# Kernel optimization log

Measured on AMD Instinct MI355X. Metric: run time of the kernel, lower is better.

Reference implementation:

```python
import jax, jax.numpy as jnp
import numpy as np

N = 150000   # nodes
E = 600000   # edges
F_IN = 32    # node features
H = 128      # hidden_channels == MLP_neurons
G = 2048     # graphs in batch


def setup_inputs() -> dict:
    key = jax.random.key(0)
    ks = iter(jax.random.split(key, 40))
    inp = {}
    inp['x'] = jax.random.normal(next(ks), (N, F_IN), dtype=jnp.float32)
    inp['edge_index'] = jax.random.randint(next(ks), (2, E), 0, N)
    inp['batch'] = jnp.sort(jax.random.randint(next(ks), (N,), 0, G))
    # GINConv MLPs: Linear(in,H) ReLU Linear(H,H) ReLU Linear(H,H)
    for i, f_in in enumerate([F_IN, H, H]):
        s1 = 1.0 / np.sqrt(f_in)
        s2 = 1.0 / np.sqrt(H)
        inp[f'c{i}_w1'] = jax.random.uniform(next(ks), (f_in, H), minval=-s1, maxval=s1)
        inp[f'c{i}_b1'] = jnp.zeros((H,), jnp.float32)
        inp[f'c{i}_w2'] = jax.random.uniform(next(ks), (H, H), minval=-s2, maxval=s2)
        inp[f'c{i}_b2'] = jnp.zeros((H,), jnp.float32)
        inp[f'c{i}_w3'] = jax.random.uniform(next(ks), (H, H), minval=-s2, maxval=s2)
        inp[f'c{i}_b3'] = jnp.zeros((H,), jnp.float32)
    s = 1.0 / np.sqrt(H)
    inp['fc0_w'] = jax.random.uniform(next(ks), (H, H), minval=-s, maxval=s)
    inp['fc0_b'] = jnp.zeros((H,), jnp.float32)
    inp['fc1_w'] = jax.random.uniform(next(ks), (H, H), minval=-s, maxval=s)
    inp['fc1_b'] = jnp.zeros((H,), jnp.float32)
    inp['out_w'] = jax.random.uniform(next(ks), (H, 2), minval=-s, maxval=s)
    inp['out_b'] = jnp.zeros((2,), jnp.float32)
    return inp


def _gin_layer(x, edge_index, w1, b1, w2, b2, w3, b3):
    # GINConv with eps=0: h = MLP(x + sum_{j in N(i)} x_j)
    agg = jax.ops.segment_sum(x[edge_index[0]], edge_index[1], num_segments=N)
    h = x + agg
    h = jax.nn.relu(h @ w1 + b1)
    h = jax.nn.relu(h @ w2 + b2)
    h = h @ w3 + b3
    return jax.nn.relu(h)  # outer .relu() in forward


def reference(x, edge_index, batch,
              c0_w1, c0_b1, c0_w2, c0_b2, c0_w3, c0_b3,
              c1_w1, c1_b1, c1_w2, c1_b2, c1_w3, c1_b3,
              c2_w1, c2_b1, c2_w2, c2_b2, c2_w3, c2_b3,
              fc0_w, fc0_b, fc1_w, fc1_b, out_w, out_b):
    h = _gin_layer(x, edge_index, c0_w1, c0_b1, c0_w2, c0_b2, c0_w3, c0_b3)
    h = _gin_layer(h, edge_index, c1_w1, c1_b1, c1_w2, c1_b2, c1_w3, c1_b3)
    h = _gin_layer(h, edge_index, c2_w1, c2_b1, c2_w2, c2_b2, c2_w3, c2_b3)
    # global_mean_pool over graph ids
    sums = jax.ops.segment_sum(h, batch, num_segments=G)            # [G,H]
    cnts = jax.ops.segment_sum(jnp.ones((N,), h.dtype), batch, num_segments=G)
    g = sums / jnp.maximum(cnts, 1.0)[:, None]
    # classifier head (dropout is identity at inference)
    g = jax.nn.relu(g @ fc0_w + fc0_b)
    g = jax.nn.relu(g @ fc1_w + fc1_b)
    return g @ out_w + out_b  # [G,2]
```

## Files before the change

kernel.cpp:

```cpp
#include <hip/hip_runtime.h>
#include <hip/hip_bf16.h>

#define NN 150000
#define EE 600000
#define F_IN 32
#define HD 128
#define GG 2048
#define CAP 28
#define NP 150016

typedef __attribute__((ext_vector_type(8))) short bf16x8;
typedef __attribute__((ext_vector_type(4))) float f32x4;

__device__ inline void split_bf16(float v, unsigned short& hi, unsigned short& lo) {
    __hip_bfloat16 h = __float2bfloat16(v);
    float hv = __bfloat162float(h);
    __hip_bfloat16 l = __float2bfloat16(v - hv);
    hi = *reinterpret_cast<unsigned short*>(&h);
    lo = *reinterpret_cast<unsigned short*>(&l);
}
__device__ inline unsigned short bf16_hi(float v) {
    __hip_bfloat16 h = __float2bfloat16(v);
    return *reinterpret_cast<unsigned short*>(&h);
}
__device__ inline float bf2f(unsigned short u) {
    union { unsigned int i; float f; } c;
    c.i = ((unsigned int)u) << 16;
    return c.f;
}

__global__ void init_zero(int* __restrict__ cnt_node, float* __restrict__ pooled) {
    int i = blockIdx.x * blockDim.x + threadIdx.x;
    if (i < NN) cnt_node[i] = 0;
    if (i < GG * HD) pooled[i] = 0.f;
}

__global__ void build_graph(const int* __restrict__ ei,
                            int* __restrict__ cnt_node,
                            int* __restrict__ bucket) {
    int e = blockIdx.x * blockDim.x + threadIdx.x;
    if (e >= EE) return;
    int src = ei[e];
    int dst = ei[EE + e];
    int slot = atomicAdd(&cnt_node[dst], 1);
    if (slot < CAP) bucket[dst * CAP + slot] = src;
}

struct PrepDesc { const float* src; unsigned short* dhi; unsigned short* dlo; int K; };
struct PrepArgs { PrepDesc d[9]; };

__global__ void prep_weights(PrepArgs pa) {
    PrepDesc de = pa.d[blockIdx.y];
    int total = de.K * HD;
    int KS = de.K >> 5;
    for (int idx = blockIdx.x * blockDim.x + threadIdx.x; idx < total;
         idx += gridDim.x * blockDim.x) {
        int k = idx / HD, h = idx - (idx / HD) * HD;
        unsigned short hi, lo;
        split_bf16(de.src[idx], hi, lo);
        int nt = h >> 4, m = h & 15;
        int ks = k >> 5, quad = (k >> 3) & 3, e = k & 7;
        int lane = quad * 16 + m;
        int pidx = ((nt * KS + ks) * 64 + lane) * 8 + e;
        de.dhi[pidx] = hi;
        de.dlo[pidx] = lo;
    }
}

template <int K_IN, bool BF16IN, bool POOL>
__launch_bounds__(128, 3)
__global__ void gin_layer(const void* __restrict__ hin_,
                          const int* __restrict__ cnt_node,
                          const int* __restrict__ bucket,
                          const unsigned short* __restrict__ w1h, const unsigned short* __restrict__ w1l,
                          const float* __restrict__ b1,
                          const unsigned short* __restrict__ w2h, const unsigned short* __restrict__ w2l,
                          const float* __restrict__ b2,
                          const unsigned short* __restrict__ w3h, const unsigned short* __restrict__ w3l,
                          const float* __restrict__ b3,
                          unsigned short* __restrict__ out,
                          const int* __restrict__ batch,
                          float* __restrict__ pooled) {
    constexpr int KS1 = K_IN / 32;
    constexpr int UN = BF16IN ? 4 : (KS1 == 1 ? 8 : 2);
    __shared__ unsigned int shp[2][2][16][128];

    const int wave = threadIdx.x >> 6;
    const int lane = threadIdx.x & 63;
    const int m = lane & 15;
    const int quad = lane >> 4;
    const int nodeBase = blockIdx.x * 64 + wave * 32;

    const float* hf = (const float*)hin_;
    const unsigned short* hb = (const unsigned short*)hin_;

    bf16x8 ah[2][KS1], al[2][KS1];
#pragma unroll
    for (int s = 0; s < 2; s++) {
        int node = nodeBase + s * 16 + m;
        node = node < NN ? node : NN - 1;
        float ag[KS1][8];
        if (BF16IN) {
            const unsigned short* rs = hb + (size_t)node * K_IN + quad * 8;
#pragma unroll
            for (int ks = 0; ks < KS1; ks++) {
                bf16x8 v = *(const bf16x8*)(rs + ks * 32);
#pragma unroll
                for (int e = 0; e < 8; e++) ag[ks][e] = bf2f((unsigned short)v[e]);
            }
        } else {
            const float* rs = hf + (size_t)node * K_IN + quad * 8;
#pragma unroll
            for (int ks = 0; ks < KS1; ks++) {
                float4 v0 = *(const float4*)(rs + ks * 32);
                float4 v1 = *(const float4*)(rs + ks * 32 + 4);
                ag[ks][0] = v0.x; ag[ks][1] = v0.y; ag[ks][2] = v0.z; ag[ks][3] = v0.w;
                ag[ks][4] = v1.x; ag[ks][5] = v1.y; ag[ks][6] = v1.z; ag[ks][7] = v1.w;
            }
        }
        int cnt = cnt_node[node];
        cnt = cnt < CAP ? cnt : CAP;
        const int* b = bucket + (size_t)node * CAP;
        int i = 0;
        if (BF16IN) {
            for (; i + UN <= cnt; i += UN) {
                bf16x8 v[UN][KS1];
#pragma unroll
                for (int j = 0; j < UN; j++) {
                    const unsigned short* r = hb + (size_t)b[i + j] * K_IN + quad * 8;
#pragma unroll
                    for (int ks = 0; ks < KS1; ks++)
                        v[j][ks] = *(const bf16x8*)(r + ks * 32);
                }
#pragma unroll
                for (int ks = 0; ks < KS1; ks++)
#pragma unroll
                    for (int e = 0; e < 8; e++) {
                        float t01 = bf2f((unsigned short)v[0][ks][e]) +
                                    bf2f((unsigned short)v[1][ks][e]);
                        float t23 = bf2f((unsigned short)v[2][ks][e]) +
                                    bf2f((unsigned short)v[3][ks][e]);
                        ag[ks][e] += t01 + t23;
                    }
            }
            for (; i < cnt; i++) {
                const unsigned short* r = hb + (size_t)b[i] * K_IN + quad * 8;
#pragma unroll
                for (int ks = 0; ks < KS1; ks++) {
                    bf16x8 v = *(const bf16x8*)(r + ks * 32);
#pragma unroll
                    for (int e = 0; e < 8; e++) ag[ks][e] += bf2f((unsigned short)v[e]);
                }
            }
        } else {
            for (; i + UN <= cnt; i += UN) {
                float4 v0[UN][KS1], v1[UN][KS1];
#pragma unroll
                for (int j = 0; j < UN; j++) {
                    const float* r = hf + (size_t)b[i + j] * K_IN + quad * 8;
#pragma unroll
                    for (int ks = 0; ks < KS1; ks++) {
                        v0[j][ks] = *(const float4*)(r + ks * 32);
                        v1[j][ks] = *(const float4*)(r + ks * 32 + 4);
                    }
                }
#pragma unroll
                for (int ks = 0; ks < KS1; ks++) {
#pragma unroll
                    for (int e = 0; e < 4; e++) {
                        float s01 = (&v0[0][ks].x)[e] + (&v0[1][ks].x)[e];
                        float s23 = (&v0[2][ks].x)[e] + (&v0[3][ks].x)[e];
                        if (UN == 8) {
                            s01 += (&v0[4][ks].x)[e] + (&v0[5][ks].x)[e];
                            s23 += (&v0[6][ks].x)[e] + (&v0[7][ks].x)[e];
                        }
                        ag[ks][e] += s01 + s23;
                    }
#pragma unroll
                    for (int e = 0; e < 4; e++) {
                        float s01 = (&v1[0][ks].x)[e] + (&v1[1][ks].x)[e];
                        float s23 = (&v1[2][ks].x)[e] + (&v1[3][ks].x)[e];
                        if (UN == 8) {
                            s01 += (&v1[4][ks].x)[e] + (&v1[5][ks].x)[e];
                            s23 += (&v1[6][ks].x)[e] + (&v1[7][ks].x)[e];
                        }
                        ag[ks][e + 4] += s01 + s23;
                    }
                }
            }
            for (; i < cnt; i++) {
                const float* r = hf + (size_t)b[i] * K_IN + quad * 8;
#pragma unroll
                for (int ks = 0; ks < KS1; ks++) {
                    float4 v0 = *(const float4*)(r + ks * 32);
                    float4 v1 = *(const float4*)(r + ks * 32 + 4);
                    ag[ks][0] += v0.x; ag[ks][1] += v0.y; ag[ks][2] += v0.z; ag[ks][3] += v0.w;
                    ag[ks][4] += v1.x; ag[ks][5] += v1.y; ag[ks][6] += v1.z; ag[ks][7] += v1.w;
                }
            }
        }
#pragma unroll
        for (int ks = 0; ks < KS1; ks++) {
            bf16x8 vh, vl;
#pragma unroll
            for (int e = 0; e < 8; e++) {
                unsigned short hi, lo;
                split_bf16(ag[ks][e], hi, lo);
                vh[e] = (short)hi;
                vl[e] = (short)lo;
            }
            ah[s][ks] = vh;
            al[s][ks] = vl;
        }
    }

    bf16x8 a2h[2][4], a2l[2][4];
    const int fxm = (m & 7) << 2;

#pragma unroll 1
    for (int nt = 0; nt < 8; nt++) {
        bf16x8 bh[KS1], bl[KS1];
#pragma unroll
        for (int ks = 0; ks < KS1; ks++) {
            bh[ks] = *(const bf16x8*)(w1h + ((nt * KS1 + ks) * 64 + lane) * 8);
            bl[ks] = *(const bf16x8*)(w1l + ((nt * KS1 + ks) * 64 + lane) * 8);
        }
        f32x4 c0 = {0.f, 0.f, 0.f, 0.f};
        f32x4 c1 = {0.f, 0.f, 0.f, 0.f};
#pragma unroll
        for (int ks = 0; ks < KS1; ks++) {
            c0 = __builtin_amdgcn_mfma_f32_16x16x32_bf16(ah[0][ks], bh[ks], c0, 0, 0, 0);
            c1 = __builtin_amdgcn_mfma_f32_16x16x32_bf16(ah[1][ks], bh[ks], c1, 0, 0, 0);
            c0 = __builtin_amdgcn_mfma_f32_16x16x32_bf16(al[0][ks], bh[ks], c0, 0, 0, 0);
            c1 = __builtin_amdgcn_mfma_f32_16x16x32_bf16(al[1][ks], bh[ks], c1, 0, 0, 0);
            c0 = __builtin_amdgcn_mfma_f32_16x16x32_bf16(ah[0][ks], bl[ks], c0, 0, 0, 0);
            c1 = __builtin_amdgcn_mfma_f32_16x16x32_bf16(ah[1][ks], bl[ks], c1, 0, 0, 0);
        }
        float bj = b1[nt * 16 + m];
#pragma unroll
        for (int r = 0; r < 4; r++) {
            int row = quad * 4 + r;
            int col = (nt * 16 + m) ^ ((row & 7) << 2);
            unsigned short hi, lo;
            split_bf16(fmaxf(c0[r] + bj, 0.f), hi, lo);
            shp[wave][0][row][col] = (unsigned int)hi | ((unsigned int)lo << 16);
            split_bf16(fmaxf(c1[r] + bj, 0.f), hi, lo);
            shp[wave][1][row][col] = (unsigned int)hi | ((unsigned int)lo << 16);
        }
    }
#pragma unroll
    for (int s = 0; s < 2; s++)
#pragma unroll
        for (int ks = 0; ks < 4; ks++) {
            const unsigned int* rowp = &shp[wave][s][m][0];
            int base = ks * 32 + quad * 8;
            uint4 wa = *(const uint4*)&rowp[base ^ fxm];
            uint4 wb = *(const uint4*)&rowp[(base + 4) ^ fxm];
            union { unsigned int u[4]; bf16x8 v; } ch, cl;
            ch.u[0] = __builtin_amdgcn_perm(wa.y, wa.x, 0x05040100u);
            ch.u[1] = __builtin_amdgcn_perm(wa.w, wa.z, 0x05040100u);
            ch.u[2] = __builtin_amdgcn_perm(wb.y, wb.x, 0x05040100u);
            ch.u[3] = __builtin_amdgcn_perm(wb.w, wb.z, 0x05040100u);
            cl.u[0] = __builtin_amdgcn_perm(wa.y, wa.x, 0x07060302u);
            cl.u[1] = __builtin_amdgcn_perm(wa.w, wa.z, 0x07060302u);
            cl.u[2] = __builtin_amdgcn_perm(wb.y, wb.x, 0x07060302u);
            cl.u[3] = __builtin_amdgcn_perm(wb.w, wb.z, 0x07060302u);
            a2h[s][ks] = ch.v;
            a2l[s][ks] = cl.v;
        }

#pragma unroll 1
    for (int nt = 0; nt < 8; nt++) {
        bf16x8 bh[4], bl[4];
#pragma unroll
        for (int ks = 0; ks < 4; ks++) {
            bh[ks] = *(const bf16x8*)(w2h + ((nt * 4 + ks) * 64 + lane) * 8);
            bl[ks] = *(const bf16x8*)(w2l + ((nt * 4 + ks) * 64 + lane) * 8);
        }
        f32x4 c0 = {0.f, 0.f, 0.f, 0.f};
        f32x4 c1 = {0.f, 0.f, 0.f, 0.f};
#pragma unroll
        for (int ks = 0; ks < 4; ks++) {
            c0 = __builtin_amdgcn_mfma_f32_16x16x32_bf16(a2h[0][ks], bh[ks], c0, 0, 0, 0);
            c1 = __builtin_amdgcn_mfma_f32_16x16x32_bf16(a2h[1][ks], bh[ks], c1, 0, 0, 0);
            c0 = __builtin_amdgcn_mfma_f32_16x16x32_bf16(a2l[0][ks], bh[ks], c0, 0, 0, 0);
            c1 = __builtin_amdgcn_mfma_f32_16x16x32_bf16(a2l[1][ks], bh[ks], c1, 0, 0, 0);
            c0 = __builtin_amdgcn_mfma_f32_16x16x32_bf16(a2h[0][ks], bl[ks], c0, 0, 0, 0);
            c1 = __builtin_amdgcn_mfma_f32_16x16x32_bf16(a2h[1][ks], bl[ks], c1, 0, 0, 0);
        }
        float bj = b2[nt * 16 + m];
#pragma unroll
        for (int r = 0; r < 4; r++) {
            int row = quad * 4 + r;
            int col = (nt * 16 + m) ^ ((row & 7) << 2);
            unsigned short hi, lo;
            split_bf16(fmaxf(c0[r] + bj, 0.f), hi, lo);
            shp[wave][0][row][col] = (unsigned int)hi | ((unsigned int)lo << 16);
            split_bf16(fmaxf(c1[r] + bj, 0.f), hi, lo);
            shp[wave][1][row][col] = (unsigned int)hi | ((unsigned int)lo << 16);
        }
    }
#pragma unroll
    for (int s = 0; s < 2; s++)
#pragma unroll
        for (int ks = 0; ks < 4; ks++) {
            const unsigned int* rowp = &shp[wave][s][m][0];
            int base = ks * 32 + quad * 8;
            uint4 wa = *(const uint4*)&rowp[base ^ fxm];
            uint4 wb = *(const uint4*)&rowp[(base + 4) ^ fxm];
            union { unsigned int u[4]; bf16x8 v; } ch, cl;
            ch.u[0] = __builtin_amdgcn_perm(wa.y, wa.x, 0x05040100u);
            ch.u[1] = __builtin_amdgcn_perm(wa.w, wa.z, 0x05040100u);
            ch.u[2] = __builtin_amdgcn_perm(wb.y, wb.x, 0x05040100u);
            ch.u[3] = __builtin_amdgcn_perm(wb.w, wb.z, 0x05040100u);
            cl.u[0] = __builtin_amdgcn_perm(wa.y, wa.x, 0x07060302u);
            cl.u[1] = __builtin_amdgcn_perm(wa.w, wa.z, 0x07060302u);
            cl.u[2] = __builtin_amdgcn_perm(wb.y, wb.x, 0x07060302u);
            cl.u[3] = __builtin_amdgcn_perm(wb.w, wb.z, 0x07060302u);
            a2h[s][ks] = ch.v;
            a2l[s][ks] = cl.v;
        }

#pragma unroll 1
    for (int nt = 0; nt < 8; nt++) {
        bf16x8 bh[4], bl[4];
#pragma unroll
        for (int ks = 0; ks < 4; ks++) {
            bh[ks] = *(const bf16x8*)(w3h + ((nt * 4 + ks) * 64 + lane) * 8);
            bl[ks] = *(const bf16x8*)(w3l + ((nt * 4 + ks) * 64 + lane) * 8);
        }
        f32x4 c0 = {0.f, 0.f, 0.f, 0.f};
        f32x4 c1 = {0.f, 0.f, 0.f, 0.f};
#pragma unroll
        for (int ks = 0; ks < 4; ks++) {
            c0 = __builtin_amdgcn_mfma_f32_16x16x32_bf16(a2h[0][ks], bh[ks], c0, 0, 0, 0);
            c1 = __builtin_amdgcn_mfma_f32_16x16x32_bf16(a2h[1][ks], bh[ks], c1, 0, 0, 0);
            c0 = __builtin_amdgcn_mfma_f32_16x16x32_bf16(a2l[0][ks], bh[ks], c0, 0, 0, 0);
            c1 = __builtin_amdgcn_mfma_f32_16x16x32_bf16(a2l[1][ks], bh[ks], c1, 0, 0, 0);
            c0 = __builtin_amdgcn_mfma_f32_16x16x32_bf16(a2h[0][ks], bl[ks], c0, 0, 0, 0);
            c1 = __builtin_amdgcn_mfma_f32_16x16x32_bf16(a2h[1][ks], bl[ks], c1, 0, 0, 0);
        }
        float bj = b3[nt * 16 + m];
        if (POOL) {
            float* shf0 = (float*)&shp[wave][0][0][0];
            float* shf1 = (float*)&shp[wave][1][0][0];
#pragma unroll
            for (int r = 0; r < 4; r++) {
                int row = quad * 4 + r;
                int col = (nt * 16 + m) ^ ((row & 7) << 2);
                shf0[row * 128 + col] = fmaxf(c0[r] + bj, 0.f);
                shf1[row * 128 + col] = fmaxf(c1[r] + bj, 0.f);
            }
        } else {
            unsigned short* t0 = (unsigned short*)&shp[wave][0][0][0];
            unsigned short* t1 = (unsigned short*)&shp[wave][1][0][0];
#pragma unroll
            for (int r = 0; r < 4; r++) {
                int row = quad * 4 + r;
                int hh = nt * 16 + m;
                int w2 = (hh >> 1) ^ ((row & 7) << 2);
                t0[row * 256 + w2 * 2 + (hh & 1)] = bf16_hi(fmaxf(c0[r] + bj, 0.f));
                t1[row * 256 + w2 * 2 + (hh & 1)] = bf16_hi(fmaxf(c1[r] + bj, 0.f));
            }
        }
    }

    if (POOL) {
#pragma unroll
        for (int h = 0; h < 2; h++) {
            float* shf = (float*)&shp[wave][h][0][0];
            int c0i = lane * 2;
            float run0 = 0.f, run1 = 0.f;
            int gp = -1;
            for (int rrow = 0; rrow < 16; rrow++) {
                int node = nodeBase + h * 16 + rrow;
                if (node >= NN) break;
                int g = batch[node];
                float2 xv = *(const float2*)&shf[rrow * 128 + (c0i ^ ((rrow & 7) << 2))];
                if (g != gp) {
                    if (gp >= 0) {
                        atomicAdd(&pooled[(size_t)gp * HD + c0i + 0], run0);
                        atomicAdd(&pooled[(size_t)gp * HD + c0i + 1], run1);
                    }
                    run0 = xv.x; run1 = xv.y; gp = g;
                } else {
                    run0 += xv.x; run1 += xv.y;
                }
            }
            if (gp >= 0) {
                atomicAdd(&pooled[(size_t)gp * HD + c0i + 0], run0);
                atomicAdd(&pooled[(size_t)gp * HD + c0i + 1], run1);
            }
        }
    } else {
#pragma unroll
        for (int s = 0; s < 2; s++) {
            unsigned short* sh16 = (unsigned short*)&shp[wave][s][0][0];
#pragma unroll
            for (int io = 0; io < 4; io++) {
                int row16 = io * 4 + quad;
                int wbase = (m * 4) ^ ((row16 & 7) << 2);
                int n2 = nodeBase + s * 16 + row16;
                bf16x8 v = *(const bf16x8*)&sh16[row16 * 256 + wbase * 2];
                if (n2 < NN) *(bf16x8*)&out[(size_t)n2 * HD + m * 8] = v;
            }
        }
    }
}

__device__ inline int lb_batch(const int* __restrict__ batch, int key) {
    int lo = 0, hi = NN;
    while (lo < hi) {
        int mid = (lo + hi) >> 1;
        if (batch[mid] < key) lo = mid + 1; else hi = mid;
    }
    return lo;
}

__launch_bounds__(128)
__global__ void head(const float* __restrict__ pooled, const int* __restrict__ batch,
                     const float* __restrict__ fc0_w, const float* __restrict__ fc0_b,
                     const float* __restrict__ fc1_w, const float* __restrict__ fc1_b,
                     const float* __restrict__ out_w, const float* __restrict__ out_b,
                     float* __restrict__ out) {
    int g = blockIdx.x;
    int j = threadIdx.x;
    __shared__ float s0[HD];
    __shared__ float s1[HD];
    int c = lb_batch(batch, g + 1) - lb_batch(batch, g);
    float cf = (float)(c > 1 ? c : 1);
    s0[j] = pooled[(size_t)g * HD + j] / cf;
    __syncthreads();

    float acc = fc0_b[j];
    for (int k = 0; k < HD; k += 4) {
        float4 hv = *(const float4*)&s0[k];
        acc = fmaf(hv.x, fc0_w[(k + 0) * HD + j], acc);
        acc = fmaf(hv.y, fc0_w[(k + 1) * HD + j], acc);
        acc = fmaf(hv.z, fc0_w[(k + 2) * HD + j], acc);
        acc = fmaf(hv.w, fc0_w[(k + 3) * HD + j], acc);
    }
    s1[j] = fmaxf(acc, 0.0f);
    __syncthreads();

    acc = fc1_b[j];
    for (int k = 0; k < HD; k += 4) {
        float4 hv = *(const float4*)&s1[k];
        acc = fmaf(hv.x, fc1_w[(k + 0) * HD + j], acc);
        acc = fmaf(hv.y, fc1_w[(k + 1) * HD + j], acc);
        acc = fmaf(hv.z, fc1_w[(k + 2) * HD + j], acc);
        acc = fmaf(hv.w, fc1_w[(k + 3) * HD + j], acc);
    }
    float v = fmaxf(acc, 0.0f);

    float p0 = v * out_w[j * 2 + 0];
    float p1 = v * out_w[j * 2 + 1];
    __syncthreads();
    s0[j] = p0;
    s1[j] = p1;
    __syncthreads();
    for (int off = 64; off >= 1; off >>= 1) {
        if (j < off) {
            s0[j] += s0[j + off];
            s1[j] += s1[j + off];
        }
        __syncthreads();
    }
    if (j == 0) {
        out[(size_t)g * 2 + 0] = s0[0] + out_b[0];
        out[(size_t)g * 2 + 1] = s1[0] + out_b[1];
    }
}

extern "C" void kernel_launch(void* const* d_in, const int* in_sizes, int n_in,
                              void* d_out, int out_size, void* d_ws, size_t ws_size,
                              hipStream_t stream) {
    const float* x     = (const float*)d_in[0];
    const int*   ei    = (const int*)d_in[1];
    const int*   batch = (const int*)d_in[2];
    const float* cw[3][6];
    for (int i = 0; i < 3; i++)
        for (int k = 0; k < 6; k++) cw[i][k] = (const float*)d_in[3 + 6 * i + k];
    const float* fc0_w = (const float*)d_in[21];
    const float* fc0_b = (const float*)d_in[22];
    const float* fc1_w = (const float*)d_in[23];
    const float* fc1_b = (const float*)d_in[24];
    const float* out_w = (const float*)d_in[25];
    const float* out_b = (const float*)d_in[26];
    float* out = (float*)d_out;

    char* ws = (char*)d_ws;
    size_t off = 0;
    auto carve = [&](size_t bytes) {
        void* p = ws + off;
        off += (bytes + 255) & ~(size_t)255;
        return p;
    };
    int*   cnt_node = (int*)carve((size_t)NN * 4);
    float* pooled   = (float*)carve((size_t)GG * HD * 4);
    int*   bucket   = (int*)carve((size_t)NN * CAP * 4);
    unsigned short* hA = (unsigned short*)carve((size_t)NP * HD * 2);
    unsigned short* hB = (unsigned short*)carve((size_t)NP * HD * 2);
    unsigned short* wHi[9];
    unsigned short* wLo[9];
    int wK[9] = {F_IN, HD, HD, HD, HD, HD, HD, HD, HD};
    for (int i = 0; i < 9; i++) {
        wHi[i] = (unsigned short*)carve((size_t)wK[i] * HD * 2);
        wLo[i] = (unsigned short*)carve((size_t)wK[i] * HD * 2);
    }
    (void)ws_size;

    init_zero<<<(GG * HD + 255) / 256, 256, 0, stream>>>(cnt_node, pooled);
    build_graph<<<(EE + 255) / 256, 256, 0, stream>>>(ei, cnt_node, bucket);

    PrepArgs pa;
    for (int l = 0; l < 3; l++)
        for (int s = 0; s < 3; s++) {
            int i = l * 3 + s;
            pa.d[i].src = cw[l][2 * s];
            pa.d[i].dhi = wHi[i];
            pa.d[i].dlo = wLo[i];
            pa.d[i].K = wK[i];
        }
    prep_weights<<<dim3(16, 9), 256, 0, stream>>>(pa);

    const int blocks = NP / 64;

    gin_layer<F_IN, false, false><<<blocks, 128, 0, stream>>>(x, cnt_node, bucket,
        wHi[0], wLo[0], cw[0][1], wHi[1], wLo[1], cw[0][3], wHi[2], wLo[2], cw[0][5],
        hA, batch, pooled);
    gin_layer<HD, true, false><<<blocks, 128, 0, stream>>>(hA, cnt_node, bucket,
        wHi[3], wLo[3], cw[1][1], wHi[4], wLo[4], cw[1][3], wHi[5], wLo[5], cw[1][5],
        hB, batch, pooled);
    gin_layer<HD, true, true><<<blocks, 128, 0, stream>>>(hB, cnt_node, bucket,
        wHi[6], wLo[6], cw[2][1], wHi[7], wLo[7], cw[2][3], wHi[8], wLo[8], cw[2][5],
        nullptr, batch, pooled);

    head<<<GG, 128, 0, stream>>>(pooled, batch, fc0_w, fc0_b, fc1_w, fc1_b, out_w, out_b, out);
}
```

Measured before the change: 527.6 us.

## Stage MLP weight slices into LDS with double-buffered async loads, 4-wave blocks

Each output-tile slice of the hi/lo bf16 weights is now copied into a double-buffered LDS area with global_load_lds, shared by four waves, instead of every wave reading the weights straight from global memory. Blocks grow from 2 to 4 waves (128 nodes per block) so the staged weights are reused by more waves. This adds a __syncthreads per output tile and doubles the LDS footprint, which may cut occupancy and add barrier stalls. The aim is to reduce redundant global and L2 weight traffic and hide load latency behind the MFMA work.

```diff
diff --git a/kernel.cpp b/kernel.cpp
--- a/kernel.cpp
+++ b/kernel.cpp
@@ -11,6 +11,8 @@
 
 typedef __attribute__((ext_vector_type(8))) short bf16x8;
 typedef __attribute__((ext_vector_type(4))) float f32x4;
+typedef __attribute__((address_space(1))) const void g1void;
+typedef __attribute__((address_space(3))) void l3void;
 
 __device__ inline void split_bf16(float v, unsigned short& hi, unsigned short& lo) {
     __hip_bfloat16 h = __float2bfloat16(v);
@@ -67,8 +69,25 @@
     }
 }
 
+template <int KS>
+__device__ inline void stage_slice(const unsigned short* __restrict__ wh,
+                                   const unsigned short* __restrict__ wl,
+                                   int nt, unsigned short* dst, int wave, int lane) {
+    if (KS == 4) {
+        const unsigned short* gh = wh + nt * 2048 + wave * 512 + lane * 8;
+        const unsigned short* gl = wl + nt * 2048 + wave * 512 + lane * 8;
+        __builtin_amdgcn_global_load_lds((g1void*)gh, (l3void*)(dst + wave * 512), 16, 0, 0);
+        __builtin_amdgcn_global_load_lds((g1void*)gl, (l3void*)(dst + 2048 + wave * 512), 16, 0, 0);
+    } else {
+        if (wave < 2) {
+            const unsigned short* g = (wave == 0 ? wh : wl) + nt * 512 + lane * 8;
+            __builtin_amdgcn_global_load_lds((g1void*)g, (l3void*)(dst + wave * 512), 16, 0, 0);
+        }
+    }
+}
+
 template <int K_IN, bool BF16IN, bool POOL>
-__launch_bounds__(128, 3)
+__launch_bounds__(256, 2)
 __global__ void gin_layer(const void* __restrict__ hin_,
                           const int* __restrict__ cnt_node,
                           const int* __restrict__ bucket,
@@ -83,13 +102,14 @@
                           float* __restrict__ pooled) {
     constexpr int KS1 = K_IN / 32;
     constexpr int UN = BF16IN ? 4 : (KS1 == 1 ? 8 : 2);
-    __shared__ unsigned int shp[2][2][16][128];
+    __shared__ unsigned int shp[4][2][16][128];
+    __shared__ unsigned short ldsW[2][4096];
 
     const int wave = threadIdx.x >> 6;
     const int lane = threadIdx.x & 63;
     const int m = lane & 15;
     const int quad = lane >> 4;
-    const int nodeBase = blockIdx.x * 64 + wave * 32;
+    const int nodeBase = blockIdx.x * 128 + wave * 32;
 
     const float* hf = (const float*)hin_;
     const unsigned short* hb = (const unsigned short*)hin_;
@@ -217,13 +237,17 @@
     bf16x8 a2h[2][4], a2l[2][4];
     const int fxm = (m & 7) << 2;
 
+    stage_slice<KS1>(w1h, w1l, 0, ldsW[0], wave, lane);
+    __syncthreads();
 #pragma unroll 1
     for (int nt = 0; nt < 8; nt++) {
+        int cur = nt & 1;
+        if (nt < 7) stage_slice<KS1>(w1h, w1l, nt + 1, ldsW[cur ^ 1], wave, lane);
         bf16x8 bh[KS1], bl[KS1];
 #pragma unroll
         for (int ks = 0; ks < KS1; ks++) {
-            bh[ks] = *(const bf16x8*)(w1h + ((nt * KS1 + ks) * 64 + lane) * 8);
-            bl[ks] = *(const bf16x8*)(w1l + ((nt * KS1 + ks) * 64 + lane) * 8);
+            bh[ks] = *(const bf16x8*)&ldsW[cur][(ks * 64 + lane) * 8];
+            bl[ks] = *(const bf16x8*)&ldsW[cur][KS1 * 512 + (ks * 64 + lane) * 8];
         }
         f32x4 c0 = {0.f, 0.f, 0.f, 0.f};
         f32x4 c1 = {0.f, 0.f, 0.f, 0.f};
@@ -247,7 +271,9 @@
             split_bf16(fmaxf(c1[r] + bj, 0.f), hi, lo);
             shp[wave][1][row][col] = (unsigned int)hi | ((unsigned int)lo << 16);
         }
-    }
+        __syncthreads();
+    }
+    stage_slice<4>(w2h, w2l, 0, ldsW[0], wave, lane);
 #pragma unroll
     for (int s = 0; s < 2; s++)
 #pragma unroll
@@ -268,14 +294,17 @@
             a2h[s][ks] = ch.v;
             a2l[s][ks] = cl.v;
         }
+    __syncthreads();
 
 #pragma unroll 1
     for (int nt = 0; nt < 8; nt++) {
+        int cur = nt & 1;
+        if (nt < 7) stage_slice<4>(w2h, w2l, nt + 1, ldsW[cur ^ 1], wave, lane);
         bf16x8 bh[4], bl[4];
 #pragma unroll
         for (int ks = 0; ks < 4; ks++) {
-            bh[ks] = *(const bf16x8*)(w2h + ((nt * 4 + ks) * 64 + lane) * 8);
-            bl[ks] = *(const bf16x8*)(w2l + ((nt * 4 + ks) * 64 + lane) * 8);
+            bh[ks] = *(const bf16x8*)&ldsW[cur][(ks * 64 + lane) * 8];
+            bl[ks] = *(const bf16x8*)&ldsW[cur][2048 + (ks * 64 + lane) * 8];
         }
         f32x4 c0 = {0.f, 0.f, 0.f, 0.f};
         f32x4 c1 = {0.f, 0.f, 0.f, 0.f};
@@ -299,7 +328,9 @@
             split_bf16(fmaxf(c1[r] + bj, 0.f), hi, lo);
             shp[wave][1][row][col] = (unsigned int)hi | ((unsigned int)lo << 16);
         }
-    }
+        __syncthreads();
+    }
+    stage_slice<4>(w3h, w3l, 0, ldsW[0], wave, lane);
 #pragma unroll
     for (int s = 0; s < 2; s++)
 #pragma unroll
@@ -320,14 +351,17 @@
             a2h[s][ks] = ch.v;
             a2l[s][ks] = cl.v;
         }
+    __syncthreads();
 
 #pragma unroll 1
     for (int nt = 0; nt < 8; nt++) {
+        int cur = nt & 1;
+        if (nt < 7) stage_slice<4>(w3h, w3l, nt + 1, ldsW[cur ^ 1], wave, lane);
         bf16x8 bh[4], bl[4];
 #pragma unroll
         for (int ks = 0; ks < 4; ks++) {
-            bh[ks] = *(const bf16x8*)(w3h + ((nt * 4 + ks) * 64 + lane) * 8);
-            bl[ks] = *(const bf16x8*)(w3l + ((nt * 4 + ks) * 64 + lane) * 8);
+            bh[ks] = *(const bf16x8*)&ldsW[cur][(ks * 64 + lane) * 8];
+            bl[ks] = *(const bf16x8*)&ldsW[cur][2048 + (ks * 64 + lane) * 8];
         }
         f32x4 c0 = {0.f, 0.f, 0.f, 0.f};
         f32x4 c1 = {0.f, 0.f, 0.f, 0.f};
@@ -363,6 +397,7 @@
                 t1[row * 256 + w2 * 2 + (hh & 1)] = bf16_hi(fmaxf(c1[r] + bj, 0.f));
             }
         }
+        __syncthreads();
     }
 
     if (POOL) {
@@ -524,15 +559,15 @@
         }
     prep_weights<<<dim3(16, 9), 256, 0, stream>>>(pa);
 
-    const int blocks = NP / 64;
-
-    gin_layer<F_IN, false, false><<<blocks, 128, 0, stream>>>(x, cnt_node, bucket,
+    const int blocks = NP / 128;
+
+    gin_layer<F_IN, false, false><<<blocks, 256, 0, stream>>>(x, cnt_node, bucket,
         wHi[0], wLo[0], cw[0][1], wHi[1], wLo[1], cw[0][3], wHi[2], wLo[2], cw[0][5],
         hA, batch, pooled);
-    gin_layer<HD, true, false><<<blocks, 128, 0, stream>>>(hA, cnt_node, bucket,
+    gin_layer<HD, true, false><<<blocks, 256, 0, stream>>>(hA, cnt_node, bucket,
         wHi[3], wLo[3], cw[1][1], wHi[4], wLo[4], cw[1][3], wHi[5], wLo[5], cw[1][5],
         hB, batch, pooled);
-    gin_layer<HD, true, true><<<blocks, 128, 0, stream>>>(hB, cnt_node, bucket,
+    gin_layer<HD, true, true><<<blocks, 256, 0, stream>>>(hB, cnt_node, bucket,
         wHi[6], wLo[6], cw[2][1], wHi[7], wLo[7], cw[2][3], wHi[8], wLo[8], cw[2][5],
         nullptr, batch, pooled);
 
```

After: 474.6 us. -10.0%, faster.
